# Kernel optimization log

Measured on AMD Instinct MI355X. Metric: run time of the kernel, lower is better.

## Reference

```python
import jax, jax.numpy as jnp
import numpy as np

EMBED_DIM = 1024
FFN_DIM = 4096
N_WIRES = 8
BATCH, SEQ = 16, 2048


def setup_inputs() -> dict:
    key = jax.random.key(0)
    ks = jax.random.split(key, 6)
    x = jax.random.normal(ks[0], (BATCH, SEQ, EMBED_DIM), dtype=jnp.float32)
    # trainable RY angles (torchquantum inits uniform in [0, 2*pi))
    theta = jax.random.uniform(ks[1], (N_WIRES,), dtype=jnp.float32) * 2.0 * jnp.pi
    # torch Linear params: W [out, in], b [out], kaiming-uniform-ish scale
    lim1 = 1.0 / np.sqrt(N_WIRES)
    W1 = jax.random.uniform(ks[2], (FFN_DIM, N_WIRES), minval=-lim1, maxval=lim1, dtype=jnp.float32)
    b1 = jax.random.uniform(ks[3], (FFN_DIM,), minval=-lim1, maxval=lim1, dtype=jnp.float32)
    lim2 = 1.0 / np.sqrt(FFN_DIM)
    W2 = jax.random.uniform(ks[4], (EMBED_DIM, FFN_DIM), minval=-lim2, maxval=lim2, dtype=jnp.float32)
    b2 = jax.random.uniform(ks[5], (EMBED_DIM,), minval=-lim2, maxval=lim2, dtype=jnp.float32)
    return {"x": x, "theta": theta, "W1": W1, "b1": b1, "W2": W2, "b2": b2}


def reference(x, theta, W1, b1, W2, b2):
    # Quantum circuit on n_wires=8 qubits: RX(x_i) encode on |0>, then RY(theta_i),
    # then <Z_i>. All gates are single-qubit on a product state, so exactly:
    #   <Z_i> = cos(x_i) * cos(theta_i)
    qz = jnp.cos(x[..., :N_WIRES]) * jnp.cos(theta)  # [B, S, 8]
    # dropout in eval mode = identity
    h = jax.nn.relu(jnp.einsum('bsw,fw->bsf', qz, W1) + b1)  # [B, S, ffn]
    out = jnp.einsum('bsf,ef->bse', h, W2) + b2  # [B, S, embed]
    return out
```

## Files before the change

### kernel.cpp

```cpp
#include <hip/hip_runtime.h>
#include <hip/hip_bf16.h>
#include <math.h>

#define EMBED 1024
#define FFN   4096
#define NW    8
#define MTOT  32768

#define BM 256
#define BN 128
#define BK 32
#define NT (FFN / BK)

#define STRIP 128
#define KPT   8

typedef __attribute__((ext_vector_type(8))) short          short8v;
typedef __attribute__((ext_vector_type(8))) unsigned short ushort8v;
typedef __attribute__((ext_vector_type(4))) float          f32x4;

typedef __attribute__((address_space(1))) void gvoid_t;
typedef __attribute__((address_space(3))) void svoid_t;

#define VMCNT(n)  asm volatile("s_waitcnt vmcnt(" #n ")" ::: "memory")
#define SCHEDB()  __builtin_amdgcn_sched_barrier(0)
#define BAR()     __builtin_amdgcn_s_barrier()

static __device__ __forceinline__ unsigned short bf16bits(float f) {
    __hip_bfloat16 h = __float2bfloat16(f);
    return *reinterpret_cast<unsigned short*>(&h);
}

__global__ __launch_bounds__(256) void cvtW2_kernel(const float* __restrict__ W2,
                                                    __hip_bfloat16* __restrict__ Bw) {
    const long i0 = ((long)blockIdx.x * 256 + threadIdx.x) * 8;
    const float4 a = *(const float4*)(W2 + i0);
    const float4 b = *(const float4*)(W2 + i0 + 4);
    float fs[8] = {a.x, a.y, a.z, a.w, b.x, b.y, b.z, b.w};
    ushort8v v;
#pragma unroll
    for (int t = 0; t < 8; ++t) v[t] = bf16bits(fs[t]);
    *reinterpret_cast<ushort8v*>(Bw + i0) = v;
}

__global__ __launch_bounds__(256) void hprod2_kernel(
    const float* __restrict__ x, const float* __restrict__ theta,
    const float* __restrict__ W1, const float* __restrict__ b1,
    __hip_bfloat16* __restrict__ h, int m0)
{
    __shared__ float qz_lds[STRIP][NW];
    const int tid   = threadIdx.x;
    const int khalf = blockIdx.x & 1;
    const int strip = blockIdx.x >> 1;
    const int k0    = khalf * 2048 + tid * KPT;

    float w1r[KPT][NW];
    float b1r[KPT];
#pragma unroll
    for (int i = 0; i < KPT; ++i) {
        const float4 a = *(const float4*)(W1 + (long)(k0 + i) * NW);
        const float4 b = *(const float4*)(W1 + (long)(k0 + i) * NW + 4);
        w1r[i][0] = a.x; w1r[i][1] = a.y; w1r[i][2] = a.z; w1r[i][3] = a.w;
        w1r[i][4] = b.x; w1r[i][5] = b.y; w1r[i][6] = b.z; w1r[i][7] = b.w;
        b1r[i] = b1[k0 + i];
    }

    if (tid < STRIP) {
        const long m = (long)m0 + (long)strip * STRIP + tid;
        const float* xr = x + m * (long)EMBED;
#pragma unroll
        for (int w = 0; w < NW; ++w)
            qz_lds[tid][w] = cosf(xr[w]) * cosf(theta[w]);
    }
    __syncthreads();

    __hip_bfloat16* hp = h + ((long)strip * STRIP) * FFN + k0;
    for (int r = 0; r < STRIP; ++r) {
        float q[NW];
#pragma unroll
        for (int w = 0; w < NW; ++w) q[w] = qz_lds[r][w];
        ushort8v hv;
#pragma unroll
        for (int i = 0; i < KPT; ++i) {
            float acc = b1r[i];
#pragma unroll
            for (int w = 0; w < NW; ++w) acc = fmaf(q[w], w1r[i][w], acc);
            hv[i] = bf16bits(fmaxf(acc, 0.0f));
        }
        *reinterpret_cast<ushort8v*>(hp + (long)r * FFN) = hv;
    }
}

__global__ __launch_bounds__(256, 2) void gemm3_kernel(
    const __hip_bfloat16* __restrict__ A,
    const __hip_bfloat16* __restrict__ Bw,
    const float* __restrict__ b2,
    float* __restrict__ out, long m0, int nPm)
{
    __shared__ __align__(16) __hip_bfloat16 As[3][BM][BK];
    __shared__ __align__(16) __hip_bfloat16 Bs[2][BN][BK];

    const int tid = threadIdx.x, wid = tid >> 6, lane = tid & 63;
    const int l15 = lane & 15, l4 = lane >> 4;
    const int wr = wid >> 1, wc = wid & 1;

    int pm, pn;
    { const int xcd = blockIdx.x & 7, k = blockIdx.x >> 3, pmx = nPm >> 3;
      pn = k / pmx; pm = xcd * pmx + (k - pn * pmx); }

    const int srow = lane >> 2;
    const int scol = (lane & 3) * 8;

    const __hip_bfloat16* Abase = A  + (long)(pm * BM + wid * 64) * FFN;
    const __hip_bfloat16* Bbase = Bw + (long)(pn * BN + wid * 32) * FFN;

    f32x4 acc[8][4];
#pragma unroll
    for (int i = 0; i < 8; ++i)
#pragma unroll
        for (int j = 0; j < 4; ++j) acc[i][j] = (f32x4){0.f, 0.f, 0.f, 0.f};

#define STAGE_A(t) do {                                                          \
    const int _b = (t) % 3;                                                      \
    const __hip_bfloat16* _g = Abase + (long)srow * FFN + (t) * BK + scol;       \
    __hip_bfloat16* _s = &As[_b][wid * 64][0];                                   \
    _Pragma("unroll")                                                            \
    for (int _gi = 0; _gi < 4; ++_gi)                                            \
        __builtin_amdgcn_global_load_lds((gvoid_t*)(_g + (long)(_gi*16)*FFN),    \
                                         (svoid_t*)(_s + _gi*16*BK), 16, 0, 0);  \
} while (0)

#define STAGE_B(t) do {                                                          \
    const int _b = (t) & 1;                                                      \
    const __hip_bfloat16* _g = Bbase + (long)srow * FFN + (t) * BK + scol;       \
    __hip_bfloat16* _s = &Bs[_b][wid * 32][0];                                   \
    _Pragma("unroll")                                                            \
    for (int _gi = 0; _gi < 2; ++_gi)                                            \
        __builtin_amdgcn_global_load_lds((gvoid_t*)(_g + (long)(_gi*16)*FFN),    \
                                         (svoid_t*)(_s + _gi*16*BK), 16, 0, 0);  \
} while (0)

    STAGE_A(0); STAGE_B(0); STAGE_A(1);

    for (int t = 0; t < NT; ++t) {
        if (t + 1 < NT) STAGE_B(t + 1);
        if (t + 2 < NT) STAGE_A(t + 2);
        if (t < NT - 2)       VMCNT(10);
        else if (t == NT - 2) VMCNT(6);
        else                  VMCNT(0);
        SCHEDB(); BAR(); SCHEDB();

        const int ba = t % 3, bb = t & 1;
        short8v bv[4], av[8];
#pragma unroll
        for (int ni = 0; ni < 4; ++ni)
            bv[ni] = *reinterpret_cast<const short8v*>(
                &Bs[bb][wc * 64 + ni * 16 + l15][l4 * 8]);
#pragma unroll
        for (int mi = 0; mi < 8; ++mi)
            av[mi] = *reinterpret_cast<const short8v*>(
                &As[ba][wr * 128 + mi * 16 + l15][l4 * 8]);

        __builtin_amdgcn_s_setprio(1);
#pragma unroll
        for (int mi = 0; mi < 8; ++mi)
#pragma unroll
            for (int ni = 0; ni < 4; ++ni)
                acc[mi][ni] = __builtin_amdgcn_mfma_f32_16x16x32_bf16(
                    av[mi], bv[ni], acc[mi][ni], 0, 0, 0);
        __builtin_amdgcn_s_setprio(0);
        SCHEDB(); BAR();
    }

#undef STAGE_A
#undef STAGE_B

    const int gn0 = pn * BN + wc * 64;
    float bias[4];
#pragma unroll
    for (int ni = 0; ni < 4; ++ni) bias[ni] = b2[gn0 + ni * 16 + l15];
    const long gm0 = m0 + (long)pm * BM + wr * 128;
#pragma unroll
    for (int mi = 0; mi < 8; ++mi)
#pragma unroll
        for (int ni = 0; ni < 4; ++ni)
#pragma unroll
            for (int j = 0; j < 4; ++j) {
                const long row = gm0 + mi * 16 + l4 * 4 + j;
                out[row * EMBED + gn0 + ni * 16 + l15] = acc[mi][ni][j] + bias[ni];
            }
}

extern "C" void kernel_launch(void* const* d_in, const int* in_sizes, int n_in,
                              void* d_out, int out_size, void* d_ws, size_t ws_size,
                              hipStream_t stream)
{
    const float* x     = (const float*)d_in[0];
    const float* theta = (const float*)d_in[1];
    const float* W1    = (const float*)d_in[2];
    const float* b1    = (const float*)d_in[3];
    const float* W2    = (const float*)d_in[4];
    const float* b2    = (const float*)d_in[5];
    float* out = (float*)d_out;

    const size_t w2b = (size_t)EMBED * FFN * 2;
    __hip_bfloat16* Bw = (__hip_bfloat16*)d_ws;
    __hip_bfloat16* h  = (__hip_bfloat16*)((char*)d_ws + w2b);
    const size_t avail = ws_size > w2b ? ws_size - w2b : 0;

    long chunk = (long)((avail / ((size_t)FFN * 2)) & ~2047UL);
    if (chunk > MTOT) chunk = MTOT;
    if (chunk < 2048) chunk = 2048;

    cvtW2_kernel<<<(EMBED * FFN) / 2048, 256, 0, stream>>>(W2, Bw);

    for (long m0 = 0; m0 < MTOT; m0 += chunk) {
        const long rows = (MTOT - m0 < chunk) ? (MTOT - m0) : chunk;
        hprod2_kernel<<<(int)((rows / STRIP) * 2), 256, 0, stream>>>(
            x, theta, W1, b1, h, (int)m0);
        const int nPm = (int)(rows / BM);
        gemm3_kernel<<<nPm * 8, 256, 0, stream>>>(h, Bw, b2, out, m0, nPm);
    }
}
```

Baseline: 414.7 us.

## Rework bf16 GEMM: 512 threads, BK=64, XOR-swizzled LDS, triple-buffered split stages

Replaces the 256-thread GEMM with a 512-thread, 8-wave version that uses a 64-wide K tile and triple-buffers both A and B in LDS. Global-to-LDS columns are XOR-swizzled to avoid bank conflicts on the reads. Each iteration is split into two MFMA halves so the next B stage is issued between them. Block-to-tile mapping changes from XCD-aware to a simple modulo, which may lose L2 locality. LDS usage roughly doubles, which risks reducing occupancy.

```diff
diff --git a/kernel.cpp b/kernel.cpp
--- a/kernel.cpp
+++ b/kernel.cpp
@@ -9,7 +9,7 @@
 
 #define BM 256
 #define BN 128
-#define BK 32
+#define BK 64
 #define NT (FFN / BK)
 
 #define STRIP 128
@@ -91,99 +91,131 @@
     }
 }
 
-__global__ __launch_bounds__(256, 2) void gemm3_kernel(
+__global__ __launch_bounds__(512, 2) void gemm4_kernel(
     const __hip_bfloat16* __restrict__ A,
     const __hip_bfloat16* __restrict__ Bw,
     const float* __restrict__ b2,
     float* __restrict__ out, long m0, int nPm)
 {
-    __shared__ __align__(16) __hip_bfloat16 As[3][BM][BK];
-    __shared__ __align__(16) __hip_bfloat16 Bs[2][BN][BK];
+    __shared__ __align__(16) __hip_bfloat16 As[3][BM * BK];
+    __shared__ __align__(16) __hip_bfloat16 Bs[3][BN * BK];
 
     const int tid = threadIdx.x, wid = tid >> 6, lane = tid & 63;
     const int l15 = lane & 15, l4 = lane >> 4;
-    const int wr = wid >> 1, wc = wid & 1;
-
-    int pm, pn;
-    { const int xcd = blockIdx.x & 7, k = blockIdx.x >> 3, pmx = nPm >> 3;
-      pn = k / pmx; pm = xcd * pmx + (k - pn * pmx); }
-
-    const int srow = lane >> 2;
-    const int scol = (lane & 3) * 8;
-
-    const __hip_bfloat16* Abase = A  + (long)(pm * BM + wid * 64) * FFN;
-    const __hip_bfloat16* Bbase = Bw + (long)(pn * BN + wid * 32) * FFN;
-
-    f32x4 acc[8][4];
+    const int wr = wid >> 2, wc = wid & 3;
+
+    const int pm = blockIdx.x % nPm, pn = blockIdx.x / nPm;
+
+    const int sr     = lane >> 3;
+    const int col_sw = ((lane & 7) ^ sr) * 8;
+
+    const __hip_bfloat16* Ag[4];
+#pragma unroll
+    for (int j = 0; j < 4; ++j)
+        Ag[j] = A + (long)(pm * BM + (wid * 4 + j) * 8 + sr) * FFN + col_sw;
+    const __hip_bfloat16* Bg[2];
+#pragma unroll
+    for (int j = 0; j < 2; ++j)
+        Bg[j] = Bw + (long)(pn * BN + (wid * 2 + j) * 8 + sr) * FFN + col_sw;
+
+    f32x4 acc[8][2];
 #pragma unroll
     for (int i = 0; i < 8; ++i)
 #pragma unroll
-        for (int j = 0; j < 4; ++j) acc[i][j] = (f32x4){0.f, 0.f, 0.f, 0.f};
-
-#define STAGE_A(t) do {                                                          \
-    const int _b = (t) % 3;                                                      \
-    const __hip_bfloat16* _g = Abase + (long)srow * FFN + (t) * BK + scol;       \
-    __hip_bfloat16* _s = &As[_b][wid * 64][0];                                   \
-    _Pragma("unroll")                                                            \
-    for (int _gi = 0; _gi < 4; ++_gi)                                            \
-        __builtin_amdgcn_global_load_lds((gvoid_t*)(_g + (long)(_gi*16)*FFN),    \
-                                         (svoid_t*)(_s + _gi*16*BK), 16, 0, 0);  \
+        for (int j = 0; j < 2; ++j) acc[i][j] = (f32x4){0.f, 0.f, 0.f, 0.f};
+
+#define STAGE_A(t) do {                                                         \
+    __hip_bfloat16* _s = &As[(t) % 3][wid * 4 * 8 * BK];                        \
+    _Pragma("unroll")                                                           \
+    for (int _j = 0; _j < 4; ++_j)                                              \
+        __builtin_amdgcn_global_load_lds((gvoid_t*)(Ag[_j] + (t) * BK),         \
+                                         (svoid_t*)(_s + _j * 8 * BK), 16, 0, 0); \
 } while (0)
 
-#define STAGE_B(t) do {                                                          \
-    const int _b = (t) & 1;                                                      \
-    const __hip_bfloat16* _g = Bbase + (long)srow * FFN + (t) * BK + scol;       \
-    __hip_bfloat16* _s = &Bs[_b][wid * 32][0];                                   \
-    _Pragma("unroll")                                                            \
-    for (int _gi = 0; _gi < 2; ++_gi)                                            \
-        __builtin_amdgcn_global_load_lds((gvoid_t*)(_g + (long)(_gi*16)*FFN),    \
-                                         (svoid_t*)(_s + _gi*16*BK), 16, 0, 0);  \
+#define STAGE_B(t) do {                                                         \
+    __hip_bfloat16* _s = &Bs[(t) % 3][wid * 2 * 8 * BK];                        \
+    _Pragma("unroll")                                                           \
+    for (int _j = 0; _j < 2; ++_j)                                              \
+        __builtin_amdgcn_global_load_lds((gvoid_t*)(Bg[_j] + (t) * BK),         \
+                                         (svoid_t*)(_s + _j * 8 * BK), 16, 0, 0); \
 } while (0)
 
-    STAGE_A(0); STAGE_B(0); STAGE_A(1);
+    STAGE_A(0); STAGE_B(0); STAGE_A(1); STAGE_B(1);
+
+    const int rxA = (l15 & 7) << 3;
 
     for (int t = 0; t < NT; ++t) {
-        if (t + 1 < NT) STAGE_B(t + 1);
+        if (t < NT - 1) { VMCNT(6); } else { VMCNT(0); }
+        SCHEDB(); BAR(); SCHEDB();
+
+        const __hip_bfloat16* as = As[t % 3];
+        const __hip_bfloat16* bs = Bs[t % 3];
+
         if (t + 2 < NT) STAGE_A(t + 2);
-        if (t < NT - 2)       VMCNT(10);
-        else if (t == NT - 2) VMCNT(6);
-        else                  VMCNT(0);
-        SCHEDB(); BAR(); SCHEDB();
-
-        const int ba = t % 3, bb = t & 1;
-        short8v bv[4], av[8];
-#pragma unroll
-        for (int ni = 0; ni < 4; ++ni)
-            bv[ni] = *reinterpret_cast<const short8v*>(
-                &Bs[bb][wc * 64 + ni * 16 + l15][l4 * 8]);
-#pragma unroll
-        for (int mi = 0; mi < 8; ++mi)
-            av[mi] = *reinterpret_cast<const short8v*>(
-                &As[ba][wr * 128 + mi * 16 + l15][l4 * 8]);
-
+
+        short8v av0[4][2], bv[2][2];
+#pragma unroll
+        for (int ni = 0; ni < 2; ++ni)
+#pragma unroll
+            for (int kk = 0; kk < 2; ++kk) {
+                const int row = wc * 32 + ni * 16 + l15;
+                bv[ni][kk] = *reinterpret_cast<const short8v*>(
+                    &bs[row * BK + ((kk * 32 + l4 * 8) ^ rxA)]);
+            }
+#pragma unroll
+        for (int mi = 0; mi < 4; ++mi)
+#pragma unroll
+            for (int kk = 0; kk < 2; ++kk) {
+                const int row = wr * 128 + mi * 16 + l15;
+                av0[mi][kk] = *reinterpret_cast<const short8v*>(
+                    &as[row * BK + ((kk * 32 + l4 * 8) ^ rxA)]);
+            }
         __builtin_amdgcn_s_setprio(1);
 #pragma unroll
-        for (int mi = 0; mi < 8; ++mi)
-#pragma unroll
-            for (int ni = 0; ni < 4; ++ni)
-                acc[mi][ni] = __builtin_amdgcn_mfma_f32_16x16x32_bf16(
-                    av[mi], bv[ni], acc[mi][ni], 0, 0, 0);
+        for (int mi = 0; mi < 4; ++mi)
+#pragma unroll
+            for (int ni = 0; ni < 2; ++ni)
+#pragma unroll
+                for (int kk = 0; kk < 2; ++kk)
+                    acc[mi][ni] = __builtin_amdgcn_mfma_f32_16x16x32_bf16(
+                        av0[mi][kk], bv[ni][kk], acc[mi][ni], 0, 0, 0);
         __builtin_amdgcn_s_setprio(0);
-        SCHEDB(); BAR();
+
+        if (t + 2 < NT) STAGE_B(t + 2);
+
+        short8v av1[4][2];
+#pragma unroll
+        for (int mi = 0; mi < 4; ++mi)
+#pragma unroll
+            for (int kk = 0; kk < 2; ++kk) {
+                const int row = wr * 128 + (mi + 4) * 16 + l15;
+                av1[mi][kk] = *reinterpret_cast<const short8v*>(
+                    &as[row * BK + ((kk * 32 + l4 * 8) ^ rxA)]);
+            }
+        __builtin_amdgcn_s_setprio(1);
+#pragma unroll
+        for (int mi = 0; mi < 4; ++mi)
+#pragma unroll
+            for (int ni = 0; ni < 2; ++ni)
+#pragma unroll
+                for (int kk = 0; kk < 2; ++kk)
+                    acc[mi + 4][ni] = __builtin_amdgcn_mfma_f32_16x16x32_bf16(
+                        av1[mi][kk], bv[ni][kk], acc[mi + 4][ni], 0, 0, 0);
+        __builtin_amdgcn_s_setprio(0);
     }
 
 #undef STAGE_A
 #undef STAGE_B
 
-    const int gn0 = pn * BN + wc * 64;
-    float bias[4];
-#pragma unroll
-    for (int ni = 0; ni < 4; ++ni) bias[ni] = b2[gn0 + ni * 16 + l15];
+    const int gn0 = pn * BN + wc * 32;
+    float bias[2];
+#pragma unroll
+    for (int ni = 0; ni < 2; ++ni) bias[ni] = b2[gn0 + ni * 16 + l15];
     const long gm0 = m0 + (long)pm * BM + wr * 128;
 #pragma unroll
     for (int mi = 0; mi < 8; ++mi)
 #pragma unroll
-        for (int ni = 0; ni < 4; ++ni)
+        for (int ni = 0; ni < 2; ++ni)
 #pragma unroll
             for (int j = 0; j < 4; ++j) {
                 const long row = gm0 + mi * 16 + l4 * 4 + j;
@@ -219,6 +251,6 @@
         hprod2_kernel<<<(int)((rows / STRIP) * 2), 256, 0, stream>>>(
             x, theta, W1, b1, h, (int)m0);
         const int nPm = (int)(rows / BM);
-        gemm3_kernel<<<nPm * 8, 256, 0, stream>>>(h, Bw, b2, out, m0, nPm);
-    }
-}
+        gemm4_kernel<<<nPm * 8, 512, 0, stream>>>(h, Bw, b2, out, m0, nPm);
+    }
+}
```

Result: slower. 594.8 us (+43.4%).

## Retile GEMM to 64x512x64 with 8 waves, XOR-swizzled LDS and single barrier

Applied to the files above, without the earlier changes.

Replaces the 256x128x32 GEMM tile with a 64x512x64 tile run by 512 threads (8 waves, each owning 64 output columns). LDS rows are XOR-swizzled to avoid bank conflicts. The loop now uses one barrier per K-step, with prefetch issued after it. Blocks map to XCDs so each XCD shares one half of W2. The goal is more reuse of the large W2 operand per block and less synchronization, at the cost of less A reuse and different occupancy and LDS pressure.

```diff
diff --git a/kernel.cpp b/kernel.cpp
--- a/kernel.cpp
+++ b/kernel.cpp
@@ -7,9 +7,9 @@
 #define NW    8
 #define MTOT  32768
 
-#define BM 256
-#define BN 128
-#define BK 32
+#define BM 64
+#define BN 512
+#define BK 64
 #define NT (FFN / BK)
 
 #define STRIP 128
@@ -91,97 +91,102 @@
     }
 }
 
-__global__ __launch_bounds__(256, 2) void gemm3_kernel(
+__global__ __launch_bounds__(512, 2) void gemm5_kernel(
     const __hip_bfloat16* __restrict__ A,
     const __hip_bfloat16* __restrict__ Bw,
     const float* __restrict__ b2,
     float* __restrict__ out, long m0, int nPm)
 {
-    __shared__ __align__(16) __hip_bfloat16 As[3][BM][BK];
-    __shared__ __align__(16) __hip_bfloat16 Bs[2][BN][BK];
+    __shared__ __align__(16) __hip_bfloat16 As[3][BM * BK];
+    __shared__ __align__(16) __hip_bfloat16 Bs[2][BN * BK];
 
     const int tid = threadIdx.x, wid = tid >> 6, lane = tid & 63;
     const int l15 = lane & 15, l4 = lane >> 4;
-    const int wr = wid >> 1, wc = wid & 1;
-
-    int pm, pn;
-    { const int xcd = blockIdx.x & 7, k = blockIdx.x >> 3, pmx = nPm >> 3;
-      pn = k / pmx; pm = xcd * pmx + (k - pn * pmx); }
-
-    const int srow = lane >> 2;
-    const int scol = (lane & 3) * 8;
-
-    const __hip_bfloat16* Abase = A  + (long)(pm * BM + wid * 64) * FFN;
-    const __hip_bfloat16* Bbase = Bw + (long)(pn * BN + wid * 32) * FFN;
-
-    f32x4 acc[8][4];
-#pragma unroll
-    for (int i = 0; i < 8; ++i)
+
+    const int xcd  = blockIdx.x & 7, slot = blockIdx.x >> 3;
+    const int pn   = xcd & 1;
+    const int pm   = (xcd >> 1) * (nPm >> 2) + slot;
+
+    const int sr    = lane >> 3;
+    const int colsw = ((lane & 7) ^ sr) * 8;
+
+    const __hip_bfloat16* Ag  = A  + (long)(pm * BM + wid * 8 + sr) * FFN + colsw;
+    const __hip_bfloat16* Bg0 = Bw + (long)(pn * BN + wid * 8 + sr) * FFN + colsw;
+
+    f32x4 acc[4][4];
+#pragma unroll
+    for (int i = 0; i < 4; ++i)
 #pragma unroll
         for (int j = 0; j < 4; ++j) acc[i][j] = (f32x4){0.f, 0.f, 0.f, 0.f};
 
-#define STAGE_A(t) do {                                                          \
-    const int _b = (t) % 3;                                                      \
-    const __hip_bfloat16* _g = Abase + (long)srow * FFN + (t) * BK + scol;       \
-    __hip_bfloat16* _s = &As[_b][wid * 64][0];                                   \
-    _Pragma("unroll")                                                            \
-    for (int _gi = 0; _gi < 4; ++_gi)                                            \
-        __builtin_amdgcn_global_load_lds((gvoid_t*)(_g + (long)(_gi*16)*FFN),    \
-                                         (svoid_t*)(_s + _gi*16*BK), 16, 0, 0);  \
+#define STAGE_A5(t) do {                                                        \
+    __builtin_amdgcn_global_load_lds((gvoid_t*)(Ag + (t) * BK),                 \
+        (svoid_t*)(&As[(t) % 3][(wid * 8) * BK]), 16, 0, 0);                    \
 } while (0)
 
-#define STAGE_B(t) do {                                                          \
-    const int _b = (t) & 1;                                                      \
-    const __hip_bfloat16* _g = Bbase + (long)srow * FFN + (t) * BK + scol;       \
-    __hip_bfloat16* _s = &Bs[_b][wid * 32][0];                                   \
-    _Pragma("unroll")                                                            \
-    for (int _gi = 0; _gi < 2; ++_gi)                                            \
-        __builtin_amdgcn_global_load_lds((gvoid_t*)(_g + (long)(_gi*16)*FFN),    \
-                                         (svoid_t*)(_s + _gi*16*BK), 16, 0, 0);  \
+#define STAGE_B5(t) do {                                                        \
+    _Pragma("unroll")                                                           \
+    for (int _j = 0; _j < 8; ++_j)                                              \
+        __builtin_amdgcn_global_load_lds(                                       \
+            (gvoid_t*)(Bg0 + (long)_j * 64 * FFN + (t) * BK),                   \
+            (svoid_t*)(&Bs[(t) & 1][(_j * 64 + wid * 8) * BK]), 16, 0, 0);      \
 } while (0)
 
-    STAGE_A(0); STAGE_B(0); STAGE_A(1);
+    STAGE_A5(0); STAGE_B5(0); STAGE_A5(1);
+
+    const int rx = (l15 & 7) << 3;
 
     for (int t = 0; t < NT; ++t) {
-        if (t + 1 < NT) STAGE_B(t + 1);
-        if (t + 2 < NT) STAGE_A(t + 2);
-        if (t < NT - 2)       VMCNT(10);
-        else if (t == NT - 2) VMCNT(6);
-        else                  VMCNT(0);
+        if (t < NT - 1) { VMCNT(1); } else { VMCNT(0); }
         SCHEDB(); BAR(); SCHEDB();
 
-        const int ba = t % 3, bb = t & 1;
-        short8v bv[4], av[8];
+        if (t + 1 < NT) STAGE_B5(t + 1);
+        if (t + 2 < NT) STAGE_A5(t + 2);
+        SCHEDB();
+
+        const __hip_bfloat16* as = As[t % 3];
+        const __hip_bfloat16* bs = Bs[t & 1];
+
+        short8v av[4][2], bv[4][2];
 #pragma unroll
         for (int ni = 0; ni < 4; ++ni)
-            bv[ni] = *reinterpret_cast<const short8v*>(
-                &Bs[bb][wc * 64 + ni * 16 + l15][l4 * 8]);
-#pragma unroll
-        for (int mi = 0; mi < 8; ++mi)
-            av[mi] = *reinterpret_cast<const short8v*>(
-                &As[ba][wr * 128 + mi * 16 + l15][l4 * 8]);
+#pragma unroll
+            for (int kk = 0; kk < 2; ++kk) {
+                const int row = wid * 64 + ni * 16 + l15;
+                bv[ni][kk] = *reinterpret_cast<const short8v*>(
+                    &bs[row * BK + ((kk * 32 + l4 * 8) ^ rx)]);
+            }
+#pragma unroll
+        for (int mi = 0; mi < 4; ++mi)
+#pragma unroll
+            for (int kk = 0; kk < 2; ++kk) {
+                const int row = mi * 16 + l15;
+                av[mi][kk] = *reinterpret_cast<const short8v*>(
+                    &as[row * BK + ((kk * 32 + l4 * 8) ^ rx)]);
+            }
 
         __builtin_amdgcn_s_setprio(1);
 #pragma unroll
-        for (int mi = 0; mi < 8; ++mi)
+        for (int mi = 0; mi < 4; ++mi)
 #pragma unroll
             for (int ni = 0; ni < 4; ++ni)
-                acc[mi][ni] = __builtin_amdgcn_mfma_f32_16x16x32_bf16(
-                    av[mi], bv[ni], acc[mi][ni], 0, 0, 0);
+#pragma unroll
+                for (int kk = 0; kk < 2; ++kk)
+                    acc[mi][ni] = __builtin_amdgcn_mfma_f32_16x16x32_bf16(
+                        av[mi][kk], bv[ni][kk], acc[mi][ni], 0, 0, 0);
         __builtin_amdgcn_s_setprio(0);
-        SCHEDB(); BAR();
-    }
-
-#undef STAGE_A
-#undef STAGE_B
-
-    const int gn0 = pn * BN + wc * 64;
+    }
+
+#undef STAGE_A5
+#undef STAGE_B5
+
+    const int gn0 = pn * BN + wid * 64;
     float bias[4];
 #pragma unroll
     for (int ni = 0; ni < 4; ++ni) bias[ni] = b2[gn0 + ni * 16 + l15];
-    const long gm0 = m0 + (long)pm * BM + wr * 128;
-#pragma unroll
-    for (int mi = 0; mi < 8; ++mi)
+    const long gm0 = m0 + (long)pm * BM;
+#pragma unroll
+    for (int mi = 0; mi < 4; ++mi)
 #pragma unroll
         for (int ni = 0; ni < 4; ++ni)
 #pragma unroll
@@ -219,6 +224,6 @@
         hprod2_kernel<<<(int)((rows / STRIP) * 2), 256, 0, stream>>>(
             x, theta, W1, b1, h, (int)m0);
         const int nPm = (int)(rows / BM);
-        gemm3_kernel<<<nPm * 8, 256, 0, stream>>>(h, Bw, b2, out, m0, nPm);
-    }
-}
+        gemm5_kernel<<<nPm * 2, 512, 0, stream>>>(h, Bw, b2, out, m0, nPm);
+    }
+}
```

After: 491.5 us. 1.19x slower.

## Restructure GEMM to 256x256x64 tiles with 8 waves and quadrant-interleaved staging

Applied to the files above, without the earlier changes.

Replaces the 256x128x32 four-wave GEMM with a 512-thread, eight-wave kernel on 256x256 tiles with BK=64. Shared-memory columns use an XOR swizzle to avoid bank conflicts. Each k-step is split into four MFMA quadrants, with the next tile's global-to-LDS loads and fragment reads interleaved between them. The aim is higher arithmetic intensity per byte loaded and better overlap of loads with MFMA, at the cost of more barriers per iteration and larger LDS use that may limit occupancy.

```diff
diff --git a/kernel.cpp b/kernel.cpp
--- a/kernel.cpp
+++ b/kernel.cpp
@@ -8,8 +8,8 @@
 #define MTOT  32768
 
 #define BM 256
-#define BN 128
-#define BK 32
+#define BN 256
+#define BK 64
 #define NT (FFN / BK)
 
 #define STRIP 128
@@ -91,28 +91,28 @@
     }
 }
 
-__global__ __launch_bounds__(256, 2) void gemm3_kernel(
+__global__ __launch_bounds__(512, 2) void gemm7_kernel(
     const __hip_bfloat16* __restrict__ A,
     const __hip_bfloat16* __restrict__ Bw,
     const float* __restrict__ b2,
     float* __restrict__ out, long m0, int nPm)
 {
-    __shared__ __align__(16) __hip_bfloat16 As[3][BM][BK];
-    __shared__ __align__(16) __hip_bfloat16 Bs[2][BN][BK];
+    __shared__ __align__(16) __hip_bfloat16 As[2][BM * BK];
+    __shared__ __align__(16) __hip_bfloat16 Bs[2][BN * BK];
 
     const int tid = threadIdx.x, wid = tid >> 6, lane = tid & 63;
     const int l15 = lane & 15, l4 = lane >> 4;
-    const int wr = wid >> 1, wc = wid & 1;
-
-    int pm, pn;
-    { const int xcd = blockIdx.x & 7, k = blockIdx.x >> 3, pmx = nPm >> 3;
-      pn = k / pmx; pm = xcd * pmx + (k - pn * pmx); }
-
-    const int srow = lane >> 2;
-    const int scol = (lane & 3) * 8;
-
-    const __hip_bfloat16* Abase = A  + (long)(pm * BM + wid * 64) * FFN;
-    const __hip_bfloat16* Bbase = Bw + (long)(pn * BN + wid * 32) * FFN;
+    const int wr = wid >> 2, wc = wid & 3;
+
+    const int xcd = blockIdx.x & 7, kb = blockIdx.x >> 3;
+    const int pn  = kb & 3;
+    const int pm  = xcd * (nPm >> 3) + (kb >> 2);
+
+    const int srow  = tid >> 3;
+    const int colsw = ((tid & 7) ^ (srow & 7)) * 8;
+
+    const __hip_bfloat16* Ag = A  + (long)(pm * BM + srow) * FFN + colsw;
+    const __hip_bfloat16* Bg = Bw + (long)(pn * BN + srow) * FFN + colsw;
 
     f32x4 acc[8][4];
 #pragma unroll
@@ -120,60 +120,85 @@
 #pragma unroll
         for (int j = 0; j < 4; ++j) acc[i][j] = (f32x4){0.f, 0.f, 0.f, 0.f};
 
-#define STAGE_A(t) do {                                                          \
-    const int _b = (t) % 3;                                                      \
-    const __hip_bfloat16* _g = Abase + (long)srow * FFN + (t) * BK + scol;       \
-    __hip_bfloat16* _s = &As[_b][wid * 64][0];                                   \
-    _Pragma("unroll")                                                            \
-    for (int _gi = 0; _gi < 4; ++_gi)                                            \
-        __builtin_amdgcn_global_load_lds((gvoid_t*)(_g + (long)(_gi*16)*FFN),    \
-                                         (svoid_t*)(_s + _gi*16*BK), 16, 0, 0);  \
+#define STAGE_A6(t, h) do {                                                     \
+    __hip_bfloat16* _s = &As[(t) & 1][((h) * 128 + wid * 8) * BK];              \
+    const __hip_bfloat16* _g = Ag + (long)((h) * 128) * FFN + (t) * BK;         \
+    __builtin_amdgcn_global_load_lds((gvoid_t*)_g, (svoid_t*)_s, 16, 0, 0);     \
+    __builtin_amdgcn_global_load_lds((gvoid_t*)(_g + (long)64 * FFN),           \
+                                     (svoid_t*)(_s + 64 * BK), 16, 0, 0);       \
 } while (0)
 
-#define STAGE_B(t) do {                                                          \
-    const int _b = (t) & 1;                                                      \
-    const __hip_bfloat16* _g = Bbase + (long)srow * FFN + (t) * BK + scol;       \
-    __hip_bfloat16* _s = &Bs[_b][wid * 32][0];                                   \
-    _Pragma("unroll")                                                            \
-    for (int _gi = 0; _gi < 2; ++_gi)                                            \
-        __builtin_amdgcn_global_load_lds((gvoid_t*)(_g + (long)(_gi*16)*FFN),    \
-                                         (svoid_t*)(_s + _gi*16*BK), 16, 0, 0);  \
+#define STAGE_B6(t, h) do {                                                     \
+    __hip_bfloat16* _s = &Bs[(t) & 1][((h) * 128 + wid * 8) * BK];              \
+    const __hip_bfloat16* _g = Bg + (long)((h) * 128) * FFN + (t) * BK;         \
+    __builtin_amdgcn_global_load_lds((gvoid_t*)_g, (svoid_t*)_s, 16, 0, 0);     \
+    __builtin_amdgcn_global_load_lds((gvoid_t*)(_g + (long)64 * FFN),           \
+                                     (svoid_t*)(_s + 64 * BK), 16, 0, 0);       \
 } while (0)
 
-    STAGE_A(0); STAGE_B(0); STAGE_A(1);
+    const int rx = (l15 & 7) << 3;
+
+    short8v aF[4][2];
+    short8v bF[2][2][2];
+
+#define READ_A6(t, a) do { _Pragma("unroll")                                    \
+    for (int mi = 0; mi < 4; ++mi) {                                            \
+        const int row = wr * 128 + (a) * 64 + mi * 16 + l15;                    \
+        _Pragma("unroll") for (int kk = 0; kk < 2; ++kk)                        \
+            aF[mi][kk] = *reinterpret_cast<const short8v*>(                     \
+                &As[(t) & 1][row * BK + ((kk * 32 + l4 * 8) ^ rx)]);            \
+    } } while (0)
+
+#define READ_B6(t, b) do { _Pragma("unroll")                                    \
+    for (int ni = 0; ni < 2; ++ni) {                                            \
+        const int row = wc * 64 + (b) * 32 + ni * 16 + l15;                     \
+        _Pragma("unroll") for (int kk = 0; kk < 2; ++kk)                        \
+            bF[b][ni][kk] = *reinterpret_cast<const short8v*>(                  \
+                &Bs[(t) & 1][row * BK + ((kk * 32 + l4 * 8) ^ rx)]);            \
+    } } while (0)
+
+#define MFMA_Q(aa, bb) do { _Pragma("unroll")                                   \
+    for (int mi = 0; mi < 4; ++mi) _Pragma("unroll")                            \
+    for (int ni = 0; ni < 2; ++ni) _Pragma("unroll")                            \
+    for (int kk = 0; kk < 2; ++kk)                                              \
+        acc[(aa) * 4 + mi][(bb) * 2 + ni] =                                     \
+            __builtin_amdgcn_mfma_f32_16x16x32_bf16(                            \
+                aF[mi][kk], bF[bb][ni][kk], acc[(aa) * 4 + mi][(bb) * 2 + ni],  \
+                0, 0, 0);                                                       \
+} while (0)
+
+    STAGE_A6(0, 0); STAGE_A6(0, 1); STAGE_B6(0, 0); STAGE_B6(0, 1);
+    STAGE_A6(1, 0);
+    VMCNT(2); SCHEDB(); BAR(); SCHEDB();
 
     for (int t = 0; t < NT; ++t) {
-        if (t + 1 < NT) STAGE_B(t + 1);
-        if (t + 2 < NT) STAGE_A(t + 2);
-        if (t < NT - 2)       VMCNT(10);
-        else if (t == NT - 2) VMCNT(6);
-        else                  VMCNT(0);
-        SCHEDB(); BAR(); SCHEDB();
-
-        const int ba = t % 3, bb = t & 1;
-        short8v bv[4], av[8];
-#pragma unroll
-        for (int ni = 0; ni < 4; ++ni)
-            bv[ni] = *reinterpret_cast<const short8v*>(
-                &Bs[bb][wc * 64 + ni * 16 + l15][l4 * 8]);
-#pragma unroll
-        for (int mi = 0; mi < 8; ++mi)
-            av[mi] = *reinterpret_cast<const short8v*>(
-                &As[ba][wr * 128 + mi * 16 + l15][l4 * 8]);
-
-        __builtin_amdgcn_s_setprio(1);
-#pragma unroll
-        for (int mi = 0; mi < 8; ++mi)
-#pragma unroll
-            for (int ni = 0; ni < 4; ++ni)
-                acc[mi][ni] = __builtin_amdgcn_mfma_f32_16x16x32_bf16(
-                    av[mi], bv[ni], acc[mi][ni], 0, 0, 0);
-        __builtin_amdgcn_s_setprio(0);
-        SCHEDB(); BAR();
-    }
-
-#undef STAGE_A
-#undef STAGE_B
+        if (t + 1 < NT) STAGE_A6(t + 1, 1);
+        READ_A6(t, 0); READ_B6(t, 0);
+        SCHEDB(); BAR(); SCHEDB();
+        __builtin_amdgcn_s_setprio(1); MFMA_Q(0, 0); __builtin_amdgcn_s_setprio(0);
+        SCHEDB(); BAR(); SCHEDB();
+        if (t + 1 < NT) STAGE_B6(t + 1, 0);
+        READ_B6(t, 1);
+        SCHEDB(); BAR(); SCHEDB();
+        __builtin_amdgcn_s_setprio(1); MFMA_Q(0, 1); __builtin_amdgcn_s_setprio(0);
+        SCHEDB(); BAR(); SCHEDB();
+        if (t + 1 < NT) STAGE_B6(t + 1, 1);
+        READ_A6(t, 1);
+        SCHEDB(); BAR(); SCHEDB();
+        __builtin_amdgcn_s_setprio(1); MFMA_Q(1, 1); __builtin_amdgcn_s_setprio(0);
+        SCHEDB(); BAR(); SCHEDB();
+        if (t + 2 < NT) STAGE_A6(t + 2, 0);
+        SCHEDB(); BAR(); SCHEDB();
+        __builtin_amdgcn_s_setprio(1); MFMA_Q(1, 0); __builtin_amdgcn_s_setprio(0);
+        if (t < NT - 2) { VMCNT(2); } else { VMCNT(0); }
+        SCHEDB(); BAR(); SCHEDB();
+    }
+
+#undef STAGE_A6
+#undef STAGE_B6
+#undef READ_A6
+#undef READ_B6
+#undef MFMA_Q
 
     const int gn0 = pn * BN + wc * 64;
     float bias[4];
@@ -219,6 +244,6 @@
         hprod2_kernel<<<(int)((rows / STRIP) * 2), 256, 0, stream>>>(
             x, theta, W1, b1, h, (int)m0);
         const int nPm = (int)(rows / BM);
-        gemm3_kernel<<<nPm * 8, 256, 0, stream>>>(h, Bw, b2, out, m0, nPm);
-    }
-}
+        gemm7_kernel<<<nPm * 4, 512, 0, stream>>>(h, Bw, b2, out, m0, nPm);
+    }
+}
```

Measured after the change: 427.3 us. 3.0% more time.
